# Kernel tuning notes

Measured on AMD Instinct MI355X. Metric: run time of the kernel, lower is better.

The kernel has to match this reference:

```python
import jax, jax.numpy as jnp
import numpy as np

B, L1, L2, D = 16, 512, 512, 512
H, INNER = 8, 1024
HD = INNER // H  # 128

def _glorot(key, shape):
    fan_in, fan_out = shape[-2], shape[-1]
    lim = jnp.sqrt(6.0 / (fan_in + fan_out))
    return jax.random.uniform(key, shape, jnp.float32, -lim, lim)

def setup_inputs() -> dict:
    key = jax.random.key(0)
    ks = jax.random.split(key, 8)
    return {
        "primary": jax.random.normal(ks[0], (B, L1, D), jnp.float32),
        "secondary": jax.random.normal(ks[1], (B, L2, D), jnp.float32),
        "primary_mask": jnp.ones((B, L1), jnp.float32),
        "secondary_mask": jnp.ones((B, L2), jnp.float32),
        "W_aff": _glorot(ks[2], (H, D, D)),          # per-head bilinear affinity weights
        "W_p": _glorot(ks[3], (D, INNER)),            # linear_primary (no bias)
        "W_s": _glorot(ks[4], (D, INNER)),            # linear_secondary (no bias)
        "W_fp": _glorot(ks[5], (D + HD, D)),          # ffn_primary
        "b_fp": jnp.zeros((D,), jnp.float32),
        "W_fs": _glorot(ks[6], (D + HD, D)),          # ffn_secondary
        "b_fs": jnp.zeros((D,), jnp.float32),
    }

def reference(primary, secondary, primary_mask, secondary_mask,
              W_aff, W_p, W_s, W_fp, b_fp, W_fs, b_fs):
    b, l1, d = primary.shape
    l2 = secondary.shape[1]
    h = W_aff.shape[0]
    hd = W_p.shape[1] // h
    # affinity mask: (B, 1, L1, L2)
    mask = (primary_mask[:, :, None] * secondary_mask[:, None, :])[:, None, :, :]
    # multi-head bilinear affinity: tanh(P Wk S^T) -> (B, H, L1, L2)
    aff = jnp.tanh(jnp.einsum('bie,hef,bjf->bhij', primary, W_aff, secondary)) * mask
    # project + split heads -> (B, H, L, hd)
    pp = (primary @ W_p).reshape(b, l1, h, hd).transpose(0, 2, 1, 3)
    ps = (secondary @ W_s).reshape(b, l2, h, hd).transpose(0, 2, 1, 3)
    # weighted sums (ReLU activation)
    wp = jax.nn.relu(jnp.einsum('bhij,bhid->bhjd', aff, pp))  # (B, H, L2, hd)
    ws = jax.nn.relu(jnp.einsum('bhij,bhjd->bhid', aff, ps))  # (B, H, L1, hd)
    # GlobalMaxPool1D applied to (L, H, hd) per sample => max over heads
    pool_p = wp.max(axis=1)  # (B, L2, hd)
    pool_s = ws.max(axis=1)  # (B, L1, hd)
    out_p = jax.nn.relu(jnp.concatenate([primary, pool_s], -1) @ W_fp + b_fp)
    out_s = jax.nn.relu(jnp.concatenate([secondary, pool_p], -1) @ W_fs + b_fs)
    return out_p, out_s
```

## Files before the change

### kernel.cpp

```cpp
#include <hip/hip_runtime.h>
#include <hip/hip_bf16.h>

typedef short short8 __attribute__((ext_vector_type(8)));
typedef float f32x16 __attribute__((ext_vector_type(16)));
typedef float f32x4 __attribute__((ext_vector_type(4)));

#define BM 128
#define BN 128

typedef const __attribute__((address_space(1))) void gas_t;
typedef __attribute__((address_space(3))) void las_t;

__device__ __forceinline__ unsigned short f2bf(float f) {
  unsigned int u = __float_as_uint(f);
  u += 0x7FFFu + ((u >> 16) & 1u);
  return (unsigned short)(u >> 16);
}

__device__ __forceinline__ float fast_tanh(float x) {
  x = fminf(fmaxf(x, -10.f), 10.f);
  float t = __builtin_amdgcn_exp2f(x * 2.8853900817779268f);
  return 1.f - 2.f * __builtin_amdgcn_rcpf(t + 1.f);
}

struct GemmP {
  const unsigned short* A;
  const unsigned short* Bm;
  void* C;
  const float* A2f;
  const unsigned short* A_b;
  const unsigned short* Bm_b;
  void* C_b;
  const float* A2f_b;
  const float* mask_p;
  const float* mask_s;
  const float* bias;
  const float* bias_b;
  long long sAb, sAh, sBb, sBh, sCb, sCh;
  int lda, lda2, ldb, ldc, M, N, K, Hh, kSplit, zSplit, nbx, nby;
};

template <int TA, int EPI>
__device__ __forceinline__ void gemm_body(const GemmP& p, int bx, int by, int bz, char* smem_) {
  constexpr int PA = (TA == 0) ? 32 : 40;
  constexpr int HSA = (TA == 0) ? 4096 : 5120;
  unsigned short* As = (unsigned short*)smem_;
  unsigned short* Bs = (unsigned short*)(smem_ + 2 * HSA * 2);

  int z = bz;
  const unsigned short* Abase = p.A;
  const unsigned short* Bbase = p.Bm;
  void* Cvp = p.C;
  const float* A2f = p.A2f;
  const float* bias = p.bias;
  if (p.zSplit && z >= p.zSplit) {
    z -= p.zSplit;
    Abase = p.A_b; Bbase = p.Bm_b; Cvp = p.C_b; A2f = p.A2f_b; bias = p.bias_b;
  }
  const int zb = z / p.Hh, zh = z % p.Hh;
  const unsigned short* A = Abase + (size_t)zb * p.sAb + (size_t)zh * p.sAh;
  const unsigned short* B = Bbase + (size_t)zb * p.sBb + (size_t)zh * p.sBh;
  const int m0 = bx * BM, n0 = by * BN;
  const int tid = threadIdx.x;
  const int wid = tid >> 6, lane = tid & 63;
  const int wm = (wid >> 1) * 64, wn = (wid & 1) * 64;
  const int lrow = lane & 31;
  const int lk8 = (lane >> 5) * 8;

  f32x16 acc[2][2] = {};

  const int dm = tid >> 2, dkg = tid & 3;

  auto mfma_block = [&]() {
#pragma unroll
    for (int h = 0; h < 2; ++h)
#pragma unroll
      for (int kc = 0; kc < 2; ++kc) {
        short8 af[2], bfv[2];
#pragma unroll
        for (int mt = 0; mt < 2; ++mt)
          af[mt] = *(const short8*)&As[h * HSA + (wm + mt * 32 + lrow) * PA + kc * 16 + lk8];
#pragma unroll
        for (int nt = 0; nt < 2; ++nt)
          bfv[nt] = *(const short8*)&Bs[h * 4096 + (wn + nt * 32 + lrow) * 32 + kc * 16 + lk8];
#pragma unroll
        for (int mt = 0; mt < 2; ++mt)
#pragma unroll
          for (int nt = 0; nt < 2; ++nt)
            acc[mt][nt] = __builtin_amdgcn_mfma_f32_32x32x16_bf16(af[mt], bfv[nt], acc[mt][nt], 0, 0, 0);
      }
  };
  auto stage_b = [&](int k0) {
#pragma unroll
    for (int h = 0; h < 2; ++h)
#pragma unroll
      for (int q = 0; q < 2; ++q) {
        const unsigned short* src = B + (size_t)(n0 + q * 64 + dm) * p.ldb + (k0 + h * 32 + dkg * 8);
        __builtin_amdgcn_global_load_lds((gas_t*)src,
                                         (las_t*)&Bs[h * 4096 + q * 2048 + wid * 512],
                                         16, 0, 0);
      }
  };

  const int nIter = p.K >> 6;
  const int nIter1 = p.kSplit ? (p.kSplit >> 6) : nIter;

  for (int it = 0; it < nIter1; ++it) {
    const int k0 = it << 6;
    if (TA == 0) {
#pragma unroll
      for (int h = 0; h < 2; ++h)
#pragma unroll
        for (int q = 0; q < 2; ++q) {
          const unsigned short* src = A + (size_t)(m0 + q * 64 + dm) * p.lda + (k0 + h * 32 + dkg * 8);
          __builtin_amdgcn_global_load_lds((gas_t*)src,
                                           (las_t*)&As[h * HSA + q * 2048 + wid * 512],
                                           16, 0, 0);
        }
    } else {
      const int kk = tid & 31, mg = (tid >> 5) << 4;
#pragma unroll
      for (int h = 0; h < 2; ++h) {
        const unsigned short* src = A + (size_t)(k0 + h * 32 + kk) * p.lda + (m0 + mg);
        uint4 v0 = *(const uint4*)src;
        uint4 v1 = *(const uint4*)(src + 8);
        unsigned short tmp[16];
        *(uint4*)&tmp[0] = v0;
        *(uint4*)&tmp[8] = v1;
#pragma unroll
        for (int j = 0; j < 16; ++j) As[h * HSA + (mg + j) * PA + kk] = tmp[j];
      }
    }
    stage_b(k0);
    __syncthreads();
    mfma_block();
    __syncthreads();
  }

  if (TA == 0 && p.kSplit) {
    for (int it = nIter1; it < nIter; ++it) {
      const int k0 = it << 6;
#pragma unroll
      for (int h = 0; h < 2; ++h) {
        const int ko = k0 + h * 32 - p.kSplit;
#pragma unroll
        for (int q = 0; q < 2; ++q) {
          const float* src = A2f + (size_t)(m0 + q * 64 + dm) * p.lda2 + (ko + dkg * 8);
          float4 v0 = *(const float4*)src;
          float4 v1 = *(const float4*)(src + 4);
          __attribute__((aligned(16))) unsigned short t[8];
          t[0] = f2bf(v0.x); t[1] = f2bf(v0.y); t[2] = f2bf(v0.z); t[3] = f2bf(v0.w);
          t[4] = f2bf(v1.x); t[5] = f2bf(v1.y); t[6] = f2bf(v1.z); t[7] = f2bf(v1.w);
          *(uint4*)&As[h * HSA + (q * 64 + dm) * 32 + dkg * 8] = *(const uint4*)t;
        }
      }
      stage_b(k0);
      __syncthreads();
      mfma_block();
      __syncthreads();
    }
  }

  unsigned short* Cu = (unsigned short*)Cvp + (size_t)zb * p.sCb + (size_t)zh * p.sCh;
  float* Cf = (float*)Cvp + (size_t)zb * p.sCb + (size_t)zh * p.sCh;

  const int rbase = 4 * (lane >> 5);

  float mp[2][16], ms[2];
  if constexpr (EPI == 1) {
#pragma unroll
    for (int mt = 0; mt < 2; ++mt)
#pragma unroll
      for (int reg = 0; reg < 16; ++reg) {
        const int rl = (reg & 3) + 8 * (reg >> 2) + rbase;
        mp[mt][reg] = p.mask_p[(size_t)zb * p.M + (m0 + wm + mt * 32 + rl)];
      }
#pragma unroll
    for (int nt = 0; nt < 2; ++nt)
      ms[nt] = p.mask_s[(size_t)zb * p.N + (n0 + wn + nt * 32 + lrow)];
  }
  if constexpr (EPI == 3) {
#pragma unroll
    for (int nt = 0; nt < 2; ++nt)
      ms[nt] = bias[n0 + wn + nt * 32 + lrow];
  }

#pragma unroll
  for (int mt = 0; mt < 2; ++mt) {
#pragma unroll
    for (int nt = 0; nt < 2; ++nt) {
      f32x16 a = acc[mt][nt];
#pragma unroll
      for (int reg = 0; reg < 16; ++reg) {
        const int rl = (reg & 3) + 8 * (reg >> 2) + rbase;
        const int grow = m0 + wm + mt * 32 + rl;
        const int gcol = n0 + wn + nt * 32 + lrow;
        const size_t idx = (size_t)grow * p.ldc + gcol;
        const float v = a[reg];
        if constexpr (EPI == 0) {
          Cu[idx] = f2bf(v);
        } else if constexpr (EPI == 1) {
          Cu[idx] = f2bf(fast_tanh(v) * (mp[mt][reg] * ms[nt]));
        } else if constexpr (EPI == 2) {
          atomicMax((int*)Cf + idx, __float_as_int(fmaxf(v, 0.f)));
        } else {
          Cf[idx] = fmaxf(v + ms[nt], 0.f);
        }
      }
    }
  }
}

template <int TA, int EPI>
__global__ __launch_bounds__(256) void gemm_k(GemmP p) {
  extern __shared__ char smem[];
  gemm_body<TA, EPI>(p, blockIdx.x, blockIdx.y, blockIdx.z, smem);
}

template <int TA1, int EPI1, int TA2, int EPI2>
__global__ __launch_bounds__(256) void gemm_pair_k(GemmP a, GemmP b, int nA) {
  extern __shared__ char smem[];
  int bid = blockIdx.x;
  if (bid < nA) {
    const int per = a.nbx * a.nby;
    const int z = bid / per, r = bid % per;
    gemm_body<TA1, EPI1>(a, r % a.nbx, r / a.nbx, z, smem);
  } else {
    bid -= nA;
    const int per = b.nbx * b.nby;
    const int z = bid / per, r = bid % per;
    gemm_body<TA2, EPI2>(b, r % b.nbx, r / b.nbx, z, smem);
  }
}

template <int EPI>
__device__ __forceinline__ void gemm11_body(const GemmP& p, int bx, int by, int bz, char* smem_) {
  int z = bz;
  const unsigned short* Abase = p.A;
  const unsigned short* Bbase = p.Bm;
  void* Cvp = p.C;
  if (p.zSplit && z >= p.zSplit) {
    z -= p.zSplit;
    Abase = p.A_b; Bbase = p.Bm_b; Cvp = p.C_b;
  }
  const int zb = z / p.Hh, zh = z % p.Hh;
  const unsigned short* A = Abase + (size_t)zb * p.sAb + (size_t)zh * p.sAh;
  const unsigned short* B = Bbase + (size_t)zb * p.sBb + (size_t)zh * p.sBh;
  const int m0 = bx * 256, n0 = by * 128;
  const int tid = threadIdx.x;
  const int wid = tid >> 6, lane = tid & 63;
  const int wm = wid >> 1, wn = wid & 1;
  const int lrow = lane & 15, lhi = lane >> 4;

  const int rr = tid >> 3;
  const int cs = ((tid & 7) * 8) ^ ((rr & 7) << 3);

  const int colx = (lhi * 16) ^ ((lrow & 7) << 4);
  const int offA = (wm * 128 + lrow) * 128 + colx;
  const int offB = 32768 + (wn * 64 + lrow) * 128 + colx;

  f32x4 acc[8][4] = {};

  const int nt = p.K >> 6;

  for (int t = 0; t < nt; ++t) {
    const int k0 = t << 6;
    const unsigned short* sa = A + (size_t)(m0 + rr) * p.lda + k0 + cs;
#pragma unroll
    for (int s = 0; s < 8; ++s)
      __builtin_amdgcn_global_load_lds((gas_t*)(sa + (size_t)(s * 32) * p.lda),
                                       (las_t*)(smem_ + s * 4096 + tid * 16), 16, 0, 0);
    const unsigned short* sb = B + (size_t)(n0 + rr) * p.ldb + k0 + cs;
#pragma unroll
    for (int s = 0; s < 4; ++s)
      __builtin_amdgcn_global_load_lds((gas_t*)(sb + (size_t)(s * 32) * p.ldb),
                                       (las_t*)(smem_ + 32768 + s * 4096 + tid * 16), 16, 0, 0);
    __syncthreads();

    short8 af[4], bv[4];
#pragma unroll
    for (int fn = 0; fn < 4; ++fn) bv[fn] = *(const short8*)(smem_ + offB + fn * 2048);
#pragma unroll
    for (int fm = 0; fm < 4; ++fm) af[fm] = *(const short8*)(smem_ + offA + fm * 2048);
    __builtin_amdgcn_s_setprio(1);
#pragma unroll
    for (int fm = 0; fm < 4; ++fm)
#pragma unroll
      for (int fn = 0; fn < 4; ++fn)
        acc[fm][fn] = __builtin_amdgcn_mfma_f32_16x16x32_bf16(af[fm], bv[fn], acc[fm][fn], 0, 0, 0);
    __builtin_amdgcn_s_setprio(0);

#pragma unroll
    for (int fm = 0; fm < 4; ++fm) af[fm] = *(const short8*)(smem_ + offA + (4 + fm) * 2048);
    __builtin_amdgcn_s_setprio(1);
#pragma unroll
    for (int fm = 0; fm < 4; ++fm)
#pragma unroll
      for (int fn = 0; fn < 4; ++fn)
        acc[4 + fm][fn] = __builtin_amdgcn_mfma_f32_16x16x32_bf16(af[fm], bv[fn], acc[4 + fm][fn], 0, 0, 0);
    __builtin_amdgcn_s_setprio(0);

#pragma unroll
    for (int fn = 0; fn < 4; ++fn) bv[fn] = *(const short8*)(smem_ + (offB ^ 64) + fn * 2048);
#pragma unroll
    for (int fm = 0; fm < 4; ++fm) af[fm] = *(const short8*)(smem_ + (offA ^ 64) + fm * 2048);
    __builtin_amdgcn_s_setprio(1);
#pragma unroll
    for (int fm = 0; fm < 4; ++fm)
#pragma unroll
      for (int fn = 0; fn < 4; ++fn)
        acc[fm][fn] = __builtin_amdgcn_mfma_f32_16x16x32_bf16(af[fm], bv[fn], acc[fm][fn], 0, 0, 0);
    __builtin_amdgcn_s_setprio(0);

#pragma unroll
    for (int fm = 0; fm < 4; ++fm) af[fm] = *(const short8*)(smem_ + (offA ^ 64) + (4 + fm) * 2048);
    __builtin_amdgcn_s_setprio(1);
#pragma unroll
    for (int fm = 0; fm < 4; ++fm)
#pragma unroll
      for (int fn = 0; fn < 4; ++fn)
        acc[4 + fm][fn] = __builtin_amdgcn_mfma_f32_16x16x32_bf16(af[fm], bv[fn], acc[4 + fm][fn], 0, 0, 0);
    __builtin_amdgcn_s_setprio(0);

    if (t + 1 < nt) __syncthreads();
  }

  unsigned short* Cu = (unsigned short*)Cvp + (size_t)zb * p.sCb + (size_t)zh * p.sCh;

  float ms[4];
  if constexpr (EPI == 1) {
#pragma unroll
    for (int fn = 0; fn < 4; ++fn)
      ms[fn] = p.mask_s[(size_t)zb * p.N + (n0 + wn * 64 + fn * 16 + lrow)];
  }

#pragma unroll
  for (int fm = 0; fm < 8; ++fm)
#pragma unroll
    for (int fn = 0; fn < 4; ++fn) {
      f32x4 a = acc[fm][fn];
      const int gcol = n0 + wn * 64 + fn * 16 + lrow;
#pragma unroll
      for (int reg = 0; reg < 4; ++reg) {
        const int grow = m0 + wm * 128 + fm * 16 + lhi * 4 + reg;
        const size_t idx = (size_t)grow * p.ldc + gcol;
        if constexpr (EPI == 0) {
          Cu[idx] = f2bf(a[reg]);
        } else {
          const float mp = p.mask_p[(size_t)zb * p.M + grow];
          Cu[idx] = f2bf(fast_tanh(a[reg]) * (mp * ms[fn]));
        }
      }
    }
}

template <int EPI>
__global__ __launch_bounds__(256, 2) void gemm11_k(GemmP p) {
  extern __shared__ char smem[];
  gemm11_body<EPI>(p, blockIdx.x, blockIdx.y, blockIdx.z, smem);
}

template <int E1, int E2>
__global__ __launch_bounds__(256, 2) void gemm11_pair_k(GemmP a, GemmP b, int nA) {
  extern __shared__ char smem[];
  int bid = blockIdx.x;
  if (bid < nA) {
    const int per = a.nbx * a.nby;
    const int z = bid / per, r = bid % per;
    gemm11_body<E1>(a, r % a.nbx, r / a.nbx, z, smem);
  } else {
    bid -= nA;
    const int per = b.nbx * b.nby;
    const int z = bid / per, r = bid % per;
    gemm11_body<E2>(b, r % b.nbx, r / b.nbx, z, smem);
  }
}

__device__ __forceinline__ void trans_body(const float* src, unsigned short* dst,
                                           int R, int C, int bx, int by, float (*tile)[33]) {
  const int r0 = by * 32, c0 = bx * 32;
  const int tx = threadIdx.x & 31, ty = threadIdx.x >> 5;
#pragma unroll
  for (int j = 0; j < 4; ++j)
    tile[ty + j * 8][tx] = src[(size_t)(r0 + ty + j * 8) * C + (c0 + tx)];
  __syncthreads();
#pragma unroll
  for (int j = 0; j < 4; ++j)
    dst[(size_t)(c0 + ty + j * 8) * R + (r0 + tx)] = f2bf(tile[tx][ty + j * 8]);
}

__global__ __launch_bounds__(256) void prep_k(const float* P, const float* S,
                                              unsigned short* Pbf, unsigned short* Sbf,
                                              const float* W_aff, unsigned short* WaT,
                                              const float* W_p, unsigned short* WpT,
                                              const float* W_s, unsigned short* WsT,
                                              const float* W_fp, unsigned short* WfpT,
                                              const float* W_fs, unsigned short* WfsT,
                                              float* poolz) {
  __shared__ float tile[32][33];
  const int bid = blockIdx.x;
  if (bid < 8192) {
    const int n4 = 1048576;
    int i = bid * 256 + threadIdx.x;
    const float4* s = (const float4*)P;
    ushort4* d = (ushort4*)Pbf;
    if (i >= n4) { i -= n4; s = (const float4*)S; d = (ushort4*)Sbf; }
    float4 v = s[i];
    ushort4 o;
    o.x = f2bf(v.x); o.y = f2bf(v.y); o.z = f2bf(v.z); o.w = f2bf(v.w);
    d[i] = o;
  } else if (bid < 10240) {
    const int l = bid - 8192;
    const int z = l >> 8, r = l & 255;
    trans_body(W_aff + (size_t)z * 262144, WaT + (size_t)z * 262144, 512, 512,
               r & 15, r >> 4, tile);
  } else if (bid < 11264) {
    const int l = bid - 10240;
    const int z = l >> 9, r = l & 511;
    trans_body(z ? W_s : W_p, z ? WsT : WpT, 512, 1024, r & 31, r >> 5, tile);
  } else if (bid < 11904) {
    const int l = bid - 11264;
    const int z = l / 320, r = l % 320;
    trans_body(z ? W_fs : W_fp, z ? WfsT : WfpT, 640, 512, r & 15, r >> 4, tile);
  } else {
    const int i = (bid - 11904) * 256 + threadIdx.x;
    ((float4*)poolz)[i] = float4{0.f, 0.f, 0.f, 0.f};
  }
}

extern "C" void kernel_launch(void* const* d_in, const int* in_sizes, int n_in,
                              void* d_out, int out_size, void* d_ws, size_t ws_size,
                              hipStream_t stream) {
  (void)in_sizes; (void)n_in; (void)out_size; (void)ws_size;
  const float* primary   = (const float*)d_in[0];
  const float* secondary = (const float*)d_in[1];
  const float* pmask     = (const float*)d_in[2];
  const float* smask     = (const float*)d_in[3];
  const float* W_aff     = (const float*)d_in[4];
  const float* W_p       = (const float*)d_in[5];
  const float* W_s       = (const float*)d_in[6];
  const float* W_fp      = (const float*)d_in[7];
  const float* b_fp      = (const float*)d_in[8];
  const float* W_fs      = (const float*)d_in[9];
  const float* b_fs      = (const float*)d_in[10];

  constexpr int Bb = 16, L = 512, Dd = 512, Hh = 8, HDd = 128, INNER = 1024, CAT = 640;
  constexpr int NT = Hh * Dd;
  constexpr long long LD = (long long)L * Dd;
  constexpr long long LL = (long long)L * L;

  static bool s_attr = [] {
    hipFuncSetAttribute(reinterpret_cast<const void*>(&gemm11_pair_k<0, 0>),
                        hipFuncAttributeMaxDynamicSharedMemorySize, 49152);
    hipFuncSetAttribute(reinterpret_cast<const void*>(&gemm11_k<1>),
                        hipFuncAttributeMaxDynamicSharedMemorySize, 49152);
    return true;
  }();
  (void)s_attr;

  char* base = (char*)d_ws;
  size_t off = 0;
  auto alloc = [&](size_t bytes) -> void* {
    void* r = base + off;
    off += (bytes + 255) & ~(size_t)255;
    return r;
  };

  unsigned short* Pbf   = (unsigned short*)alloc((size_t)Bb * L * Dd * 2);
  unsigned short* Sbf   = (unsigned short*)alloc((size_t)Bb * L * Dd * 2);
  unsigned short* WaT   = (unsigned short*)alloc((size_t)NT * Dd * 2);
  unsigned short* WpT   = (unsigned short*)alloc((size_t)INNER * Dd * 2);
  unsigned short* WsT   = (unsigned short*)alloc((size_t)INNER * Dd * 2);
  unsigned short* WfpT  = (unsigned short*)alloc((size_t)Dd * CAT * 2);
  unsigned short* WfsT  = (unsigned short*)alloc((size_t)Dd * CAT * 2);
  unsigned short* psT   = (unsigned short*)alloc((size_t)Bb * INNER * L * 2);
  unsigned short* ppT   = (unsigned short*)alloc((size_t)Bb * INNER * L * 2);
  unsigned short* Tbuf  = (unsigned short*)alloc((size_t)Bb * L * NT * 2);
  unsigned short* affb  = (unsigned short*)alloc((size_t)Bb * Hh * L * L * 2);
  float* pool_p = (float*)alloc((size_t)Bb * L * HDd * 4);
  float* pool_s = (float*)alloc((size_t)Bb * L * HDd * 4);

  prep_k<<<dim3(13952), dim3(256), 0, stream>>>(primary, secondary, Pbf, Sbf,
                                                W_aff, WaT, W_p, WpT, W_s, WsT,
                                                W_fp, WfpT, W_fs, WfsT, pool_p);

  {
    GemmP a{};
    a.A = Pbf; a.lda = Dd;
    a.Bm = WaT; a.ldb = Dd;
    a.C = Tbuf; a.ldc = NT;
    a.M = Bb * L; a.N = NT; a.K = Dd; a.Hh = 1; a.nbx = 32; a.nby = 32;

    GemmP b{};
    b.A = WsT; b.lda = Dd; b.sAb = 0;
    b.Bm = Sbf; b.ldb = Dd; b.sBb = LD;
    b.C = psT; b.ldc = L; b.sCb = (long long)INNER * L;
    b.A_b = WpT; b.Bm_b = Pbf; b.C_b = ppT;
    b.M = INNER; b.N = L; b.K = Dd; b.Hh = 1; b.zSplit = Bb; b.nbx = 4; b.nby = 4;

    gemm11_pair_k<0, 0><<<dim3(1024 + 512), dim3(256), 49152, stream>>>(a, b, 1024);
  }

  {
    GemmP g{};
    g.A = Tbuf; g.lda = NT; g.sAb = (long long)L * NT; g.sAh = Dd;
    g.Bm = Sbf; g.ldb = Dd; g.sBb = LD; g.sBh = 0;
    g.C = affb; g.ldc = L; g.sCb = (long long)Hh * LL; g.sCh = LL;
    g.mask_p = pmask; g.mask_s = smask;
    g.M = L; g.N = L; g.K = Dd; g.Hh = Hh;
    gemm11_k<1><<<dim3(2, 4, Bb * Hh), dim3(256), 49152, stream>>>(g);
  }

  {
    GemmP g4{};
    g4.A = affb; g4.lda = L; g4.sAb = (long long)Hh * LL; g4.sAh = LL;
    g4.Bm = psT; g4.ldb = L; g4.sBb = (long long)INNER * L; g4.sBh = (long long)HDd * L;
    g4.C = pool_s; g4.ldc = HDd; g4.sCb = (long long)L * HDd; g4.sCh = 0;
    g4.M = L; g4.N = HDd; g4.K = L; g4.Hh = Hh; g4.nbx = 4; g4.nby = 1;

    GemmP g5 = g4;
    g5.Bm = ppT;
    g5.C = pool_p;

    gemm_pair_k<0, 2, 1, 2><<<dim3(512 + 512), dim3(256), 36864, stream>>>(g4, g5, 512);
  }

  {
    GemmP g{};
    g.A = Pbf; g.lda = Dd;
    g.A2f = pool_s; g.lda2 = HDd; g.kSplit = Dd;
    g.Bm = WfpT; g.ldb = CAT;
    g.C = d_out; g.ldc = Dd;
    g.bias = b_fp;
    g.A_b = Sbf; g.A2f_b = pool_p; g.Bm_b = WfsT;
    g.C_b = (float*)d_out + (size_t)Bb * L * Dd;
    g.bias_b = b_fs;
    g.M = Bb * L; g.N = Dd; g.K = CAT; g.Hh = 1; g.zSplit = 1;
    gemm_k<0, 3><<<dim3(64, 4, 2), dim3(256), 32768, stream>>>(g);
  }
}
```

Measured before the change: 322.4 us.

## Replace atomicMax head pooling with bf16 per-head stores and a separate reduce kernel

The weighted-sum GEMMs now write ReLU'd per-head results as bf16 into a scratch buffer (reusing Tbuf) instead of doing fp32 atomicMax into pooled outputs. A new reduce kernel takes the max over the 8 heads, two bf16 values at a time, and widens the result to fp32. This also drops the zero-init of the pool buffers from the prep kernel. It trades global atomic contention for an extra kernel launch and a round trip through memory, and pooled values are now rounded to bf16.

```diff
diff --git a/kernel.cpp b/kernel.cpp
--- a/kernel.cpp
+++ b/kernel.cpp
@@ -203,8 +203,10 @@
           Cu[idx] = f2bf(fast_tanh(v) * (mp[mt][reg] * ms[nt]));
         } else if constexpr (EPI == 2) {
           atomicMax((int*)Cf + idx, __float_as_int(fmaxf(v, 0.f)));
+        } else if constexpr (EPI == 3) {
+          Cf[idx] = fmaxf(v + ms[nt], 0.f);
         } else {
-          Cf[idx] = fmaxf(v + ms[nt], 0.f);
+          Cu[idx] = f2bf(fmaxf(v, 0.f));
         }
       }
     }
@@ -376,6 +378,29 @@
   }
 }
 
+__global__ __launch_bounds__(256) void reduce_k(const unsigned int* ws, const unsigned int* wp,
+                                                float* pool_s, float* pool_p) {
+  int t = blockIdx.x * 256 + threadIdx.x;
+  const unsigned int* src = ws;
+  float* dst = pool_s;
+  if (t >= 524288) { t -= 524288; src = wp; dst = pool_p; }
+  const int o2 = t * 2;
+  const int b = o2 >> 16, r = o2 & 65535;
+  const unsigned int* s = src + (((size_t)b * 524288 + r) >> 1);
+  unsigned int m = s[0];
+#pragma unroll
+  for (int h = 1; h < 8; ++h) {
+    const unsigned int v = s[h * 32768];
+    const unsigned int lo = (v & 0xFFFFu) > (m & 0xFFFFu) ? (v & 0xFFFFu) : (m & 0xFFFFu);
+    const unsigned int hi = (v >> 16) > (m >> 16) ? (v & 0xFFFF0000u) : (m & 0xFFFF0000u);
+    m = lo | hi;
+  }
+  float2 o;
+  o.x = __uint_as_float((m & 0xFFFFu) << 16);
+  o.y = __uint_as_float(m & 0xFFFF0000u);
+  *(float2*)&dst[o2] = o;
+}
+
 __device__ __forceinline__ void trans_body(const float* src, unsigned short* dst,
                                            int R, int C, int bx, int by, float (*tile)[33]) {
   const int r0 = by * 32, c0 = bx * 32;
@@ -395,8 +420,7 @@
                                               const float* W_p, unsigned short* WpT,
                                               const float* W_s, unsigned short* WsT,
                                               const float* W_fp, unsigned short* WfpT,
-                                              const float* W_fs, unsigned short* WfsT,
-                                              float* poolz) {
+                                              const float* W_fs, unsigned short* WfsT) {
   __shared__ float tile[32][33];
   const int bid = blockIdx.x;
   if (bid < 8192) {
@@ -418,13 +442,10 @@
     const int l = bid - 10240;
     const int z = l >> 9, r = l & 511;
     trans_body(z ? W_s : W_p, z ? WsT : WpT, 512, 1024, r & 31, r >> 5, tile);
-  } else if (bid < 11904) {
+  } else {
     const int l = bid - 11264;
     const int z = l / 320, r = l % 320;
     trans_body(z ? W_fs : W_fp, z ? WfsT : WfpT, 640, 512, r & 15, r >> 4, tile);
-  } else {
-    const int i = (bid - 11904) * 256 + threadIdx.x;
-    ((float4*)poolz)[i] = float4{0.f, 0.f, 0.f, 0.f};
   }
 }
 
@@ -480,9 +501,12 @@
   float* pool_p = (float*)alloc((size_t)Bb * L * HDd * 4);
   float* pool_s = (float*)alloc((size_t)Bb * L * HDd * 4);
 
-  prep_k<<<dim3(13952), dim3(256), 0, stream>>>(primary, secondary, Pbf, Sbf,
+  unsigned short* wsBuf = Tbuf;
+  unsigned short* wpBuf = Tbuf + (size_t)Bb * Hh * L * HDd;
+
+  prep_k<<<dim3(11904), dim3(256), 0, stream>>>(primary, secondary, Pbf, Sbf,
                                                 W_aff, WaT, W_p, WpT, W_s, WsT,
-                                                W_fp, WfpT, W_fs, WfsT, pool_p);
+                                                W_fp, WfpT, W_fs, WfsT);
 
   {
     GemmP a{};
@@ -515,15 +539,19 @@
     GemmP g4{};
     g4.A = affb; g4.lda = L; g4.sAb = (long long)Hh * LL; g4.sAh = LL;
     g4.Bm = psT; g4.ldb = L; g4.sBb = (long long)INNER * L; g4.sBh = (long long)HDd * L;
-    g4.C = pool_s; g4.ldc = HDd; g4.sCb = (long long)L * HDd; g4.sCh = 0;
+    g4.C = wsBuf; g4.ldc = HDd; g4.sCb = (long long)Hh * L * HDd; g4.sCh = (long long)L * HDd;
     g4.M = L; g4.N = HDd; g4.K = L; g4.Hh = Hh; g4.nbx = 4; g4.nby = 1;
 
     GemmP g5 = g4;
     g5.Bm = ppT;
-    g5.C = pool_p;
-
-    gemm_pair_k<0, 2, 1, 2><<<dim3(512 + 512), dim3(256), 36864, stream>>>(g4, g5, 512);
-  }
+    g5.C = wpBuf;
+
+    gemm_pair_k<0, 4, 1, 4><<<dim3(512 + 512), dim3(256), 36864, stream>>>(g4, g5, 512);
+  }
+
+  reduce_k<<<dim3(4096), dim3(256), 0, stream>>>((const unsigned int*)wsBuf,
+                                                 (const unsigned int*)wpBuf,
+                                                 pool_s, pool_p);
 
   {
     GemmP g{};
```

After: 307.1 us. 4.8% less time.

## Write per-head ReLU outputs as bf16 and fold head max-pool into FFN A-load

Applied to the files above, without the earlier changes.

Removes the float atomicMax head-pooling epilogue and the zero-init of the pool buffers. The weighted-sum GEMMs now write per-head ReLU results as bf16 planes into the reused Tbuf. The final FFN kernel then takes the max over the 8 heads while loading its A operand, using packed unsigned 16-bit compares, which are valid because ReLU outputs are non-negative. One weighted-sum GEMM is moved to the larger 256-row tile kernel through a mixed pair launcher, and launch bounds are raised to 3 blocks per SM. The cost is 8x more reads in the FFN's pooled-operand load and extra bf16 plane writes, plus hard-coded plane strides.

```diff
diff --git a/kernel.cpp b/kernel.cpp
--- a/kernel.cpp
+++ b/kernel.cpp
@@ -15,6 +15,12 @@
   unsigned int u = __float_as_uint(f);
   u += 0x7FFFu + ((u >> 16) & 1u);
   return (unsigned short)(u >> 16);
+}
+
+__device__ __forceinline__ unsigned int pmaxu16(unsigned int a, unsigned int b) {
+  unsigned int lo = ((a & 0xFFFFu) > (b & 0xFFFFu)) ? (a & 0xFFFFu) : (b & 0xFFFFu);
+  unsigned int hi = ((a >> 16) > (b >> 16)) ? (a & 0xFFFF0000u) : (b & 0xFFFF0000u);
+  return lo | hi;
 }
 
 __device__ __forceinline__ float fast_tanh(float x) {
@@ -138,20 +144,27 @@
   }
 
   if (TA == 0 && p.kSplit) {
+    const unsigned short* planes = (const unsigned short*)A2f;
     for (int it = nIter1; it < nIter; ++it) {
       const int k0 = it << 6;
 #pragma unroll
-      for (int h = 0; h < 2; ++h) {
-        const int ko = k0 + h * 32 - p.kSplit;
+      for (int h2 = 0; h2 < 2; ++h2) {
+        const int ko = k0 + h2 * 32 - p.kSplit;
 #pragma unroll
         for (int q = 0; q < 2; ++q) {
-          const float* src = A2f + (size_t)(m0 + q * 64 + dm) * p.lda2 + (ko + dkg * 8);
-          float4 v0 = *(const float4*)src;
-          float4 v1 = *(const float4*)(src + 4);
-          __attribute__((aligned(16))) unsigned short t[8];
-          t[0] = f2bf(v0.x); t[1] = f2bf(v0.y); t[2] = f2bf(v0.z); t[3] = f2bf(v0.w);
-          t[4] = f2bf(v1.x); t[5] = f2bf(v1.y); t[6] = f2bf(v1.z); t[7] = f2bf(v1.w);
-          *(uint4*)&As[h * HSA + (q * 64 + dm) * 32 + dkg * 8] = *(const uint4*)t;
+          const int row = m0 + q * 64 + dm;
+          const unsigned int* s0 = (const unsigned int*)(planes
+              + ((size_t)(((row >> 9) << 12) + (row & 511)) * 128 + ko + dkg * 8));
+          uint4 mv = *(const uint4*)s0;
+#pragma unroll
+          for (int hh = 1; hh < 8; ++hh) {
+            uint4 v = *(const uint4*)(s0 + (size_t)hh * 32768);
+            mv.x = pmaxu16(mv.x, v.x);
+            mv.y = pmaxu16(mv.y, v.y);
+            mv.z = pmaxu16(mv.z, v.z);
+            mv.w = pmaxu16(mv.w, v.w);
+          }
+          *(uint4*)&As[h2 * HSA + (q * 64 + dm) * 32 + dkg * 8] = mv;
         }
       }
       stage_b(k0);
@@ -201,10 +214,10 @@
           Cu[idx] = f2bf(v);
         } else if constexpr (EPI == 1) {
           Cu[idx] = f2bf(fast_tanh(v) * (mp[mt][reg] * ms[nt]));
-        } else if constexpr (EPI == 2) {
-          atomicMax((int*)Cf + idx, __float_as_int(fmaxf(v, 0.f)));
+        } else if constexpr (EPI == 3) {
+          Cf[idx] = fmaxf(v + ms[nt], 0.f);
         } else {
-          Cf[idx] = fmaxf(v + ms[nt], 0.f);
+          Cu[idx] = f2bf(fmaxf(v, 0.f));
         }
       }
     }
@@ -215,22 +228,6 @@
 __global__ __launch_bounds__(256) void gemm_k(GemmP p) {
   extern __shared__ char smem[];
   gemm_body<TA, EPI>(p, blockIdx.x, blockIdx.y, blockIdx.z, smem);
-}
-
-template <int TA1, int EPI1, int TA2, int EPI2>
-__global__ __launch_bounds__(256) void gemm_pair_k(GemmP a, GemmP b, int nA) {
-  extern __shared__ char smem[];
-  int bid = blockIdx.x;
-  if (bid < nA) {
-    const int per = a.nbx * a.nby;
-    const int z = bid / per, r = bid % per;
-    gemm_body<TA1, EPI1>(a, r % a.nbx, r / a.nbx, z, smem);
-  } else {
-    bid -= nA;
-    const int per = b.nbx * b.nby;
-    const int z = bid / per, r = bid % per;
-    gemm_body<TA2, EPI2>(b, r % b.nbx, r / b.nbx, z, smem);
-  }
 }
 
 template <int EPI>
@@ -346,6 +343,8 @@
         const size_t idx = (size_t)grow * p.ldc + gcol;
         if constexpr (EPI == 0) {
           Cu[idx] = f2bf(a[reg]);
+        } else if constexpr (EPI == 4) {
+          Cu[idx] = f2bf(fmaxf(a[reg], 0.f));
         } else {
           const float mp = p.mask_p[(size_t)zb * p.M + grow];
           Cu[idx] = f2bf(fast_tanh(a[reg]) * (mp * ms[fn]));
@@ -355,13 +354,13 @@
 }
 
 template <int EPI>
-__global__ __launch_bounds__(256, 2) void gemm11_k(GemmP p) {
+__global__ __launch_bounds__(256, 3) void gemm11_k(GemmP p) {
   extern __shared__ char smem[];
   gemm11_body<EPI>(p, blockIdx.x, blockIdx.y, blockIdx.z, smem);
 }
 
 template <int E1, int E2>
-__global__ __launch_bounds__(256, 2) void gemm11_pair_k(GemmP a, GemmP b, int nA) {
+__global__ __launch_bounds__(256, 3) void gemm11_pair_k(GemmP a, GemmP b, int nA) {
   extern __shared__ char smem[];
   int bid = blockIdx.x;
   if (bid < nA) {
@@ -376,6 +375,22 @@
   }
 }
 
+template <int E1, int TA2, int E2>
+__global__ __launch_bounds__(256, 3) void mix_pair_k(GemmP a, GemmP b, int nA) {
+  extern __shared__ char smem[];
+  int bid = blockIdx.x;
+  if (bid < nA) {
+    const int per = a.nbx * a.nby;
+    const int z = bid / per, r = bid % per;
+    gemm11_body<E1>(a, r % a.nbx, r / a.nbx, z, smem);
+  } else {
+    bid -= nA;
+    const int per = b.nbx * b.nby;
+    const int z = bid / per, r = bid % per;
+    gemm_body<TA2, E2>(b, r % b.nbx, r / b.nbx, z, smem);
+  }
+}
+
 __device__ __forceinline__ void trans_body(const float* src, unsigned short* dst,
                                            int R, int C, int bx, int by, float (*tile)[33]) {
   const int r0 = by * 32, c0 = bx * 32;
@@ -395,8 +410,7 @@
                                               const float* W_p, unsigned short* WpT,
                                               const float* W_s, unsigned short* WsT,
                                               const float* W_fp, unsigned short* WfpT,
-                                              const float* W_fs, unsigned short* WfsT,
-                                              float* poolz) {
+                                              const float* W_fs, unsigned short* WfsT) {
   __shared__ float tile[32][33];
   const int bid = blockIdx.x;
   if (bid < 8192) {
@@ -418,13 +432,10 @@
     const int l = bid - 10240;
     const int z = l >> 9, r = l & 511;
     trans_body(z ? W_s : W_p, z ? WsT : WpT, 512, 1024, r & 31, r >> 5, tile);
-  } else if (bid < 11904) {
+  } else {
     const int l = bid - 11264;
     const int z = l / 320, r = l % 320;
     trans_body(z ? W_fs : W_fp, z ? WfsT : WfpT, 640, 512, r & 15, r >> 4, tile);
-  } else {
-    const int i = (bid - 11904) * 256 + threadIdx.x;
-    ((float4*)poolz)[i] = float4{0.f, 0.f, 0.f, 0.f};
   }
 }
 
@@ -454,6 +465,8 @@
                         hipFuncAttributeMaxDynamicSharedMemorySize, 49152);
     hipFuncSetAttribute(reinterpret_cast<const void*>(&gemm11_k<1>),
                         hipFuncAttributeMaxDynamicSharedMemorySize, 49152);
+    hipFuncSetAttribute(reinterpret_cast<const void*>(&mix_pair_k<4, 1, 4>),
+                        hipFuncAttributeMaxDynamicSharedMemorySize, 49152);
     return true;
   }();
   (void)s_attr;
@@ -477,12 +490,13 @@
   unsigned short* ppT   = (unsigned short*)alloc((size_t)Bb * INNER * L * 2);
   unsigned short* Tbuf  = (unsigned short*)alloc((size_t)Bb * L * NT * 2);
   unsigned short* affb  = (unsigned short*)alloc((size_t)Bb * Hh * L * L * 2);
-  float* pool_p = (float*)alloc((size_t)Bb * L * HDd * 4);
-  float* pool_s = (float*)alloc((size_t)Bb * L * HDd * 4);
-
-  prep_k<<<dim3(13952), dim3(256), 0, stream>>>(primary, secondary, Pbf, Sbf,
+
+  unsigned short* wsBuf = Tbuf;
+  unsigned short* wpBuf = Tbuf + (size_t)Bb * Hh * L * HDd;
+
+  prep_k<<<dim3(11904), dim3(256), 0, stream>>>(primary, secondary, Pbf, Sbf,
                                                 W_aff, WaT, W_p, WpT, W_s, WsT,
-                                                W_fp, WfpT, W_fs, WfsT, pool_p);
+                                                W_fp, WfpT, W_fs, WfsT);
 
   {
     GemmP a{};
@@ -512,27 +526,29 @@
   }
 
   {
-    GemmP g4{};
-    g4.A = affb; g4.lda = L; g4.sAb = (long long)Hh * LL; g4.sAh = LL;
-    g4.Bm = psT; g4.ldb = L; g4.sBb = (long long)INNER * L; g4.sBh = (long long)HDd * L;
-    g4.C = pool_s; g4.ldc = HDd; g4.sCb = (long long)L * HDd; g4.sCh = 0;
-    g4.M = L; g4.N = HDd; g4.K = L; g4.Hh = Hh; g4.nbx = 4; g4.nby = 1;
-
-    GemmP g5 = g4;
-    g5.Bm = ppT;
-    g5.C = pool_p;
-
-    gemm_pair_k<0, 2, 1, 2><<<dim3(512 + 512), dim3(256), 36864, stream>>>(g4, g5, 512);
+    GemmP a{};
+    a.A = affb; a.lda = L; a.sAb = (long long)Hh * LL; a.sAh = LL;
+    a.Bm = psT; a.ldb = L; a.sBb = (long long)INNER * L; a.sBh = (long long)HDd * L;
+    a.C = wsBuf; a.ldc = HDd; a.sCb = (long long)Hh * L * HDd; a.sCh = (long long)L * HDd;
+    a.M = L; a.N = HDd; a.K = L; a.Hh = Hh; a.nbx = 2; a.nby = 1;
+
+    GemmP b{};
+    b.A = affb; b.lda = L; b.sAb = (long long)Hh * LL; b.sAh = LL;
+    b.Bm = ppT; b.ldb = L; b.sBb = (long long)INNER * L; b.sBh = (long long)HDd * L;
+    b.C = wpBuf; b.ldc = HDd; b.sCb = (long long)Hh * L * HDd; b.sCh = (long long)L * HDd;
+    b.M = L; b.N = HDd; b.K = L; b.Hh = Hh; b.nbx = 4; b.nby = 1;
+
+    mix_pair_k<4, 1, 4><<<dim3(256 + 512), dim3(256), 49152, stream>>>(a, b, 256);
   }
 
   {
     GemmP g{};
     g.A = Pbf; g.lda = Dd;
-    g.A2f = pool_s; g.lda2 = HDd; g.kSplit = Dd;
+    g.A2f = (const float*)wsBuf; g.lda2 = HDd; g.kSplit = Dd;
     g.Bm = WfpT; g.ldb = CAT;
     g.C = d_out; g.ldc = Dd;
     g.bias = b_fp;
-    g.A_b = Sbf; g.A2f_b = pool_p; g.Bm_b = WfsT;
+    g.A_b = Sbf; g.A2f_b = (const float*)wpBuf; g.Bm_b = WfsT;
     g.C_b = (float*)d_out + (size_t)Bb * L * Dd;
     g.bias_b = b_fs;
     g.M = Bb * L; g.N = Dd; g.K = CAT; g.Hh = 1; g.zSplit = 1;
```

Result: slower. 366.7 us (+13.7%).
